# Performance work log

Hardware: AMD Instinct MI355X
Metric: run time of the kernel (lower is better)

## Reference

```python
import jax, jax.numpy as jnp
import numpy as np

B, C, H, W = 16, 512, 64, 64

def setup_inputs() -> dict:
    key = jax.random.key(0)
    k1, k2, k3 = jax.random.split(key, 3)
    x = jax.random.normal(k1, (B, C, H, W), dtype=jnp.float32)
    gamma = jnp.zeros((1,), dtype=jnp.float32)
    W1 = jax.random.normal(k2, (C, C // 8), dtype=jnp.float32) * (1.0 / np.sqrt(C))
    b1 = jnp.zeros((C // 8,), dtype=jnp.float32)
    W2 = jax.random.normal(k3, (C // 8, C), dtype=jnp.float32) * (1.0 / np.sqrt(C // 8))
    b2 = jnp.zeros((C,), dtype=jnp.float32)
    return {"x": x, "gamma": gamma, "W1": W1, "b1": b1, "W2": W2, "b2": b2}

def reference(x, gamma, W1, b1, W2, b2):
    b, c, h, w = x.shape
    q = x.reshape(b, c, h * w)                      # B,C,HW
    energy = jnp.einsum('bcn,bdn->bcd', q, q)       # B,C,C
    energy_new = jnp.max(energy, axis=-1, keepdims=True) - energy
    attention = jax.nn.softmax(energy_new, axis=-1)
    ch_out = jnp.einsum('bcd,bdn->bcn', attention, q).reshape(b, c, h, w)
    # SE branch: global avg pool -> Linear -> ReLU -> Linear -> Sigmoid
    se = jnp.mean(x, axis=(2, 3))                   # B,C
    se = jax.nn.relu(se @ W1 + b1)
    se = jax.nn.sigmoid(se @ W2 + b2)               # B,C
    out = gamma * (ch_out * se[:, :, None, None]) + x
    return out
```

## Files before the change

kernel.cpp:

```cpp
#include <hip/hip_runtime.h>
#include <cstdint>
#include <cstddef>

#define B_ 16
#define C_ 512
#define N_ 4096
#define CH_ 64

#define VMWAIT(n) asm volatile("s_waitcnt vmcnt(" #n ")" ::: "memory")
#define BARRAW()  asm volatile("s_barrier" ::: "memory")

typedef __attribute__((ext_vector_type(8))) short short8;
typedef __attribute__((ext_vector_type(4))) short short4t;
typedef __attribute__((ext_vector_type(4))) float f32x4;

__device__ __forceinline__ unsigned short f2bf(float f) {
  union { float f; unsigned u; } v; v.f = f;
  unsigned r = v.u + 0x7FFFu + ((v.u >> 16) & 1u);
  return (unsigned short)(r >> 16);
}
__device__ __forceinline__ ushort4 cvt4(float4 v) {
  ushort4 u; u.x = f2bf(v.x); u.y = f2bf(v.y); u.z = f2bf(v.z); u.w = f2bf(v.w);
  return u;
}
__device__ __forceinline__ void gload_lds16(const void* g, void* l) {
  __builtin_amdgcn_global_load_lds((__attribute__((address_space(1))) void*)g,
                                   (__attribute__((address_space(3))) void*)l,
                                   16, 0, 0);
}
__device__ __forceinline__ unsigned lds_off(const void* p) {
  return (unsigned)(size_t)(__attribute__((address_space(3))) const char*)p;
}

template <int CPW>
__device__ __forceinline__ void stage_pair(
    const unsigned short* __restrict__ Asrc, const unsigned short* __restrict__ Bsrc,
    char* Adst, char* Bdst, int t, int ko, bool doB) {
  const int l = t & 63, wid = t >> 6;
  const int srow = l >> 3, scc = l & 7;
#pragma unroll
  for (int i = 0; i < CPW; ++i) {
    const int chunk = wid * CPW + i;
    const int row = chunk * 8 + srow;
    const int cc = scc ^ (row & 7);
    gload_lds16(Asrc + (size_t)row * N_ + ko + cc * 8, Adst + chunk * 1024);
    if (doB)
      gload_lds16(Bsrc + (size_t)row * N_ + ko + cc * 8, Bdst + chunk * 1024);
  }
}
__device__ __forceinline__ void stage_att(
    const unsigned short* __restrict__ src, char* dst, int t, int ko) {
  const int l = t & 63, wid = t >> 6;
  const int srow = l >> 3, scc = l & 7;
#pragma unroll
  for (int i = 0; i < 2; ++i) {
    const int chunk = wid * 2 + i;
    const int row = chunk * 8 + srow;
    const int cc = scc ^ (row & 7);
    gload_lds16(src + (size_t)row * C_ + ko + cc * 8, dst + chunk * 1024);
  }
}
__device__ __forceinline__ void stage_q(
    const unsigned short* __restrict__ src,
    char* dst, int t) {
  const int l = t & 63, wid = t >> 6;
  const int dd = (l >> 1) & 3;
  const int n8 = ((l >> 3) << 1) | (l & 1);
#pragma unroll
  for (int i = 0; i < 2; ++i) {
    const int chunk = wid * 2 + i;
    gload_lds16(src + (size_t)(4 * chunk + dd) * N_ + n8 * 8,
                dst + chunk * 1024);
  }
}

template <int MF, int NF>
__device__ __forceinline__ void gemm_step_t(const char* Abase, const char* Bbase,
                                            int l, int wA, int wB,
                                            f32x4 (&acc)[MF][NF]) {
#pragma unroll
  for (int ks = 0; ks < 2; ++ks) {
    short8 af[MF], bfv[NF];
#pragma unroll
    for (int m = 0; m < MF; ++m) {
      const int row = wA * (MF * 16) + m * 16 + (l & 15);
      const int ch = (ks * 4 + (l >> 4)) ^ (row & 7);
      af[m] = *(const short8*)(Abase + row * 128 + ch * 16);
    }
#pragma unroll
    for (int n = 0; n < NF; ++n) {
      const int row = wB * (NF * 16) + n * 16 + (l & 15);
      const int ch = (ks * 4 + (l >> 4)) ^ (row & 7);
      bfv[n] = *(const short8*)(Bbase + row * 128 + ch * 16);
    }
#pragma unroll
    for (int m = 0; m < MF; ++m)
#pragma unroll
      for (int n = 0; n < NF; ++n)
        acc[m][n] = __builtin_amdgcn_mfma_f32_16x16x32_bf16(af[m], bfv[n],
                                                            acc[m][n], 0, 0, 0);
  }
}

__device__ __forceinline__ void gemm_tr(const char* Q, const char* P,
                                        int l, int wn, int wcc,
                                        f32x4 (&acc)[2][4]) {
  const int g = l >> 4;
  const unsigned qoff = lds_off(Q) + g * 2048 + (l & 15) * 2;
#pragma unroll
  for (int ks = 0; ks < 2; ++ks) {
    short4t alo[2], ahi[2];
#pragma unroll
    for (int m = 0; m < 2; ++m) {
      const unsigned a = qoff + ks * 8192 + (wn * 2 + m) * 128;
      asm volatile("ds_read_b64_tr_b16 %0, %2\n\t"
                   "ds_read_b64_tr_b16 %1, %2 offset:1024"
                   : "=&v"(alo[m]), "=&v"(ahi[m]) : "v"(a));
    }
    short8 bfv[4];
#pragma unroll
    for (int n = 0; n < 4; ++n) {
      const int row = wcc * 64 + n * 16 + (l & 15);
      const int ch = (ks * 4 + (l >> 4)) ^ (row & 7);
      bfv[n] = *(const short8*)(P + row * 128 + ch * 16);
    }
    asm volatile("s_waitcnt lgkmcnt(0)" ::: "memory");
    __builtin_amdgcn_sched_barrier(0);
#pragma unroll
    for (int m = 0; m < 2; ++m) {
      short8 af = __builtin_shufflevector(alo[m], ahi[m], 0, 1, 2, 3, 4, 5, 6, 7);
#pragma unroll
      for (int n = 0; n < 4; ++n)
        acc[m][n] = __builtin_amdgcn_mfma_f32_16x16x32_bf16(af, bfv[n],
                                                            acc[m][n], 0, 0, 0);
    }
  }
}

__global__ __launch_bounds__(256) void k1_convert(
    const float* __restrict__ x, unsigned short* __restrict__ qbf,
    float* __restrict__ partial) {
  __shared__ float wsum[4];
  const size_t base = (size_t)blockIdx.x * N_;
  const int t = threadIdx.x;
  float s = 0.f;
#pragma unroll
  for (int k = 0; k < 4; ++k) {
    const int idx = (t + k * 256) * 4;
    float4 v = *(const float4*)(x + base + idx);
    *(ushort4*)(qbf + base + idx) = cvt4(v);
    s += (v.x + v.y) + (v.z + v.w);
  }
#pragma unroll
  for (int o = 1; o < 64; o <<= 1) s += __shfl_xor(s, o);
  if ((t & 63) == 0) wsum[t >> 6] = s;
  __syncthreads();
  if (t == 0) partial[blockIdx.x] = (wsum[0] + wsum[1]) + (wsum[2] + wsum[3]);
}

__global__ __launch_bounds__(256) void k2_se(
    const float* __restrict__ partial, const float* __restrict__ gamma,
    const float* __restrict__ W1, const float* __restrict__ b1,
    const float* __restrict__ W2, const float* __restrict__ b2,
    float* __restrict__ gse) {
  __shared__ float se_s[C_];
  __shared__ float hp[4][CH_];
  __shared__ float h_s[CH_];
  const int b = blockIdx.x, t = threadIdx.x;
  for (int c = t; c < C_; c += 256)
    se_s[c] = partial[b * C_ + c] * (1.0f / (float)N_);
  __syncthreads();
  {
    const int h = t & 63, seg = t >> 6;
    float a = 0.f;
    const int cb = seg * 128;
    for (int c = cb; c < cb + 128; ++c) a += se_s[c] * W1[c * CH_ + h];
    hp[seg][h] = a;
  }
  __syncthreads();
  if (t < CH_) {
    float a = b1[t] + hp[0][t] + hp[1][t] + hp[2][t] + hp[3][t];
    h_s[t] = fmaxf(a, 0.f);
  }
  __syncthreads();
  const float g = gamma[0];
  for (int c = t; c < C_; c += 256) {
    float a = b2[c];
#pragma unroll
    for (int hh = 0; hh < CH_; ++hh) a += h_s[hh] * W2[hh * C_ + c];
    const float sig = 1.0f / (1.0f + __expf(-a));
    gse[b * C_ + c] = g * sig;
  }
}

__global__ __launch_bounds__(512) void k3_energy(
    const unsigned short* __restrict__ qbf, float* __restrict__ ep) {
  __shared__ alignas(16) char lds[65536];
  const int orig = blockIdx.x;
  const int wg = (orig & 7) * 80 + (orig >> 3);
  const int b = wg / 40;
  const int rem = wg % 40;
  const int kc = rem / 10;
  const int tid = rem % 10;
  int i, j;
  if (tid < 4)      { i = 0; j = tid; }
  else if (tid < 7) { i = 1; j = tid - 3; }
  else if (tid < 9) { i = 2; j = tid - 5; }
  else              { i = 3; j = 3; }
  const int c0 = i * 128, d0 = j * 128;
  const bool diag = (i == j);
  const unsigned short* qb = qbf + (size_t)b * C_ * N_ + kc * 1024;
  const int t = threadIdx.x, l = t & 63, wid = t >> 6;
  const int wd = wid >> 1, wcc = wid & 1;
  f32x4 acc[2][4];
#pragma unroll
  for (int m = 0; m < 2; ++m)
#pragma unroll
    for (int n = 0; n < 4; ++n) acc[m][n] = (f32x4){0.f, 0.f, 0.f, 0.f};
  char* A0 = lds;             char* B0 = lds + 16384;
  char* A1 = lds + 32768;     char* B1 = lds + 49152;
  const unsigned short* cp = qb + (size_t)c0 * N_;
  const unsigned short* dp = qb + (size_t)d0 * N_;

  stage_pair<2>(cp, dp, A0, B0, t, 0, !diag);
  for (int kt = 0; kt < 16; ++kt) {
    char* curA = (kt & 1) ? A1 : A0;
    char* curB = (kt & 1) ? B1 : B0;
    char* nxtA = (kt & 1) ? A0 : A1;
    char* nxtB = (kt & 1) ? B0 : B1;
    if (kt < 15) {
      stage_pair<2>(cp, dp, nxtA, nxtB, t, (kt + 1) * 64, !diag);
      if (diag) { VMWAIT(2); } else { VMWAIT(4); }
    } else {
      VMWAIT(0);
    }
    BARRAW();
    gemm_step_t<2, 4>(diag ? curA : curB, curA, l, wd, wcc, acc);
    BARRAW();
  }

  float* Lf = (float*)lds;
  float* eb = ep + ((size_t)(kc * B_ + b)) * C_ * C_;
#pragma unroll
  for (int df = 0; df < 2; ++df)
#pragma unroll
    for (int cf = 0; cf < 4; ++cf) {
      const int c_l = wcc * 64 + cf * 16 + (l & 15);
      const int d4 = wd * 32 + df * 16 + ((l >> 4) << 2);
      *(float4*)&Lf[c_l * 128 + (d4 ^ ((c_l & 7) << 2))] =
          *(const float4*)&acc[df][cf];
    }
  __syncthreads();
#pragma unroll
  for (int jj = 0; jj < 8; ++jj) {
    const int row = jj * 16 + (t >> 5);
    const int col4 = (t & 31) * 4;
    float4 v = *(const float4*)&Lf[row * 128 + (col4 ^ ((row & 7) << 2))];
    *(float4*)&eb[(size_t)(c0 + row) * C_ + d0 + col4] = v;
  }
  if (!diag) {
    __syncthreads();
#pragma unroll
    for (int df = 0; df < 2; ++df)
#pragma unroll
      for (int cf = 0; cf < 4; ++cf) {
        const int c_l = wcc * 64 + cf * 16 + (l & 15);
#pragma unroll
        for (int r = 0; r < 4; ++r) {
          const int d_l = wd * 32 + df * 16 + ((l >> 4) << 2) + r;
          Lf[d_l * 128 + (c_l ^ ((d_l & 7) << 2))] = acc[df][cf][r];
        }
      }
    __syncthreads();
#pragma unroll
    for (int jj = 0; jj < 8; ++jj) {
      const int row = jj * 16 + (t >> 5);
      const int col4 = (t & 31) * 4;
      float4 v = *(const float4*)&Lf[row * 128 + (col4 ^ ((row & 7) << 2))];
      *(float4*)&eb[(size_t)(d0 + row) * C_ + c0 + col4] = v;
    }
  }
}

__global__ __launch_bounds__(256) void k4_softmax(const float* __restrict__ ep,
                                                  unsigned short* __restrict__ att) {
  const int t = threadIdx.x, l = t & 63, wid = t >> 6;
  const size_t row = (size_t)blockIdx.x * 4 + wid;
  f32x4 v0 = (f32x4){0.f, 0.f, 0.f, 0.f}, v1 = v0;
#pragma unroll
  for (int k = 0; k < 4; ++k) {
    const f32x4* er = (const f32x4*)(ep + ((size_t)k * B_ * C_ + row) * C_);
    v0 += er[l];
    v1 += er[64 + l];
  }
  float mn = fminf(fminf(fminf(v0[0], v0[1]), fminf(v0[2], v0[3])),
                   fminf(fminf(v1[0], v1[1]), fminf(v1[2], v1[3])));
#pragma unroll
  for (int s = 1; s < 64; s <<= 1) mn = fminf(mn, __shfl_xor(mn, s));
  float e0 = __expf(mn - v0[0]), e1 = __expf(mn - v0[1]);
  float e2 = __expf(mn - v0[2]), e3 = __expf(mn - v0[3]);
  float e4 = __expf(mn - v1[0]), e5 = __expf(mn - v1[1]);
  float e6 = __expf(mn - v1[2]), e7 = __expf(mn - v1[3]);
  float sm = ((e0 + e1) + (e2 + e3)) + ((e4 + e5) + (e6 + e7));
#pragma unroll
  for (int s = 1; s < 64; s <<= 1) sm += __shfl_xor(sm, s);
  const float inv = 1.0f / sm;
  unsigned short* ar = att + row * C_;
  ushort4 u0, u1;
  u0.x = f2bf(e0 * inv); u0.y = f2bf(e1 * inv);
  u0.z = f2bf(e2 * inv); u0.w = f2bf(e3 * inv);
  u1.x = f2bf(e4 * inv); u1.y = f2bf(e5 * inv);
  u1.z = f2bf(e6 * inv); u1.w = f2bf(e7 * inv);
  *(ushort4*)(ar + 4 * l) = u0;
  *(ushort4*)(ar + 256 + 4 * l) = u1;
}

__global__ __launch_bounds__(512) void k5_pv(
    const unsigned short* __restrict__ att, const unsigned short* __restrict__ qbf,
    const float* __restrict__ gse, const float* __restrict__ x,
    float* __restrict__ out) {
  __shared__ alignas(16) char lds[65536];
  const int orig = blockIdx.x;
  const int wg = (orig & 7) * 256 + (orig >> 3);
  const int b = wg >> 7;
  const int rem = wg & 127;
  const int c0 = (rem & 3) * 128, n0 = (rem >> 2) * 128;
  const int t = threadIdx.x, l = t & 63, wid = t >> 6;
  const int wn = wid >> 1, wcc = wid & 1;
  const unsigned short* ap = att + (size_t)b * C_ * C_ + (size_t)c0 * C_;
  const unsigned short* qb = qbf + (size_t)b * C_ * N_ + n0;
  f32x4 acc[2][4];
#pragma unroll
  for (int m = 0; m < 2; ++m)
#pragma unroll
    for (int n = 0; n < 4; ++n) acc[m][n] = (f32x4){0.f, 0.f, 0.f, 0.f};
  char* P0 = lds;             char* Q0 = lds + 16384;
  char* P1 = lds + 32768;     char* Q1 = lds + 49152;

  stage_att(ap, P0, t, 0);
  stage_q(qb, Q0, t);
  for (int kt = 0; kt < 8; ++kt) {
    char* curP = (kt & 1) ? P1 : P0;
    char* curQ = (kt & 1) ? Q1 : Q0;
    char* nxtP = (kt & 1) ? P0 : P1;
    char* nxtQ = (kt & 1) ? Q0 : Q1;
    if (kt < 7) {
      stage_att(ap, nxtP, t, (kt + 1) * 64);
      stage_q(qb + (size_t)(kt + 1) * 64 * N_, nxtQ, t);
      VMWAIT(4);
    } else {
      VMWAIT(0);
    }
    BARRAW();
    gemm_tr(curQ, curP, l, wn, wcc, acc);
    BARRAW();
  }

  float* Lf = (float*)lds;
#pragma unroll
  for (int nf = 0; nf < 2; ++nf)
#pragma unroll
    for (int cf = 0; cf < 4; ++cf) {
      const int c_l = wcc * 64 + cf * 16 + (l & 15);
      const int n4 = wn * 32 + nf * 16 + ((l >> 4) << 2);
      *(float4*)&Lf[c_l * 128 + (n4 ^ ((c_l & 7) << 2))] =
          *(const float4*)&acc[nf][cf];
    }
  __syncthreads();
  const float* xb = x + (size_t)b * C_ * N_;
  float* ob = out + (size_t)b * C_ * N_;
  const float* gseb = gse + b * C_;
#pragma unroll
  for (int jj = 0; jj < 8; ++jj) {
    const int row = jj * 16 + (t >> 5);
    const int col4 = (t & 31) * 4;
    const int c = c0 + row;
    const float g = gseb[c];
    float4 v = *(const float4*)&Lf[row * 128 + (col4 ^ ((row & 7) << 2))];
    const size_t gofs = (size_t)c * N_ + n0 + col4;
    float4 xv = *(const float4*)(xb + gofs);
    float4 ov;
    ov.x = g * v.x + xv.x; ov.y = g * v.y + xv.y;
    ov.z = g * v.z + xv.z; ov.w = g * v.w + xv.w;
    *(float4*)(ob + gofs) = ov;
  }
}

extern "C" void kernel_launch(void* const* d_in, const int* in_sizes, int n_in,
                              void* d_out, int out_size, void* d_ws, size_t ws_size,
                              hipStream_t stream) {
  (void)in_sizes; (void)n_in; (void)out_size; (void)ws_size;
  const float* x     = (const float*)d_in[0];
  const float* gamma = (const float*)d_in[1];
  const float* W1    = (const float*)d_in[2];
  const float* b1    = (const float*)d_in[3];
  const float* W2    = (const float*)d_in[4];
  const float* b2    = (const float*)d_in[5];
  float* out = (float*)d_out;
  char* ws = (char*)d_ws;

  unsigned short* qbf     = (unsigned short*)(ws);
  unsigned short* att     = (unsigned short*)(ws + 67108864);
  float*          partial = (float*)(ws + 75497472);
  float*          gse     = (float*)(ws + 75530240);
  float* epartial = out;

  k1_convert<<<dim3(B_ * C_), dim3(256), 0, stream>>>(x, qbf, partial);
  k2_se<<<dim3(B_), dim3(256), 0, stream>>>(partial, gamma, W1, b1, W2, b2, gse);
  k3_energy<<<dim3(640), dim3(512), 0, stream>>>(qbf, epartial);
  k4_softmax<<<dim3(B_ * C_ / 4), dim3(256), 0, stream>>>(epartial, att);
  k5_pv<<<dim3(2048), dim3(512), 0, stream>>>(att, qbf, gse, x, out);
}
```

Before: 204.4 us.

## Enlarge PV tile to 256x256 with phased MFMA schedule and bf16 residual

Each k5_pv workgroup now computes a 256x256 output tile instead of 128x128. The grid drops to 512 blocks, LDS doubles to 128KB, and each K step is split into four phases that interleave transposed LDS reads, MFMA bursts at raised priority, and barriers. This is meant to improve reuse of attention and Q tiles and cut global staging traffic. The epilogue now takes the residual from the bf16 copy of x instead of the fp32 input, which halves that read but lowers the residual's precision. The larger accumulator array raises register pressure, and the bigger LDS footprint limits residency to one block per CU.

```diff
diff --git a/kernel.cpp b/kernel.cpp
--- a/kernel.cpp
+++ b/kernel.cpp
@@ -8,6 +8,7 @@
 #define CH_ 64
 
 #define VMWAIT(n) asm volatile("s_waitcnt vmcnt(" #n ")" ::: "memory")
+#define LGKM0()   asm volatile("s_waitcnt lgkmcnt(0)" ::: "memory")
 #define BARRAW()  asm volatile("s_barrier" ::: "memory")
 
 typedef __attribute__((ext_vector_type(8))) short short8;
@@ -18,6 +19,10 @@
   union { float f; unsigned u; } v; v.f = f;
   unsigned r = v.u + 0x7FFFu + ((v.u >> 16) & 1u);
   return (unsigned short)(r >> 16);
+}
+__device__ __forceinline__ float bf2f(unsigned short u) {
+  union { unsigned u; float f; } v; v.u = ((unsigned)u) << 16;
+  return v.f;
 }
 __device__ __forceinline__ ushort4 cvt4(float4 v) {
   ushort4 u; u.x = f2bf(v.x); u.y = f2bf(v.y); u.z = f2bf(v.z); u.w = f2bf(v.w);
@@ -48,93 +53,112 @@
       gload_lds16(Bsrc + (size_t)row * N_ + ko + cc * 8, Bdst + chunk * 1024);
   }
 }
-__device__ __forceinline__ void stage_att(
+template <int MF, int NF>
+__device__ __forceinline__ void gemm_step_t(const char* Abase, const char* Bbase,
+                                            int l, int wA, int wB,
+                                            f32x4 (&acc)[MF][NF]) {
+#pragma unroll
+  for (int ks = 0; ks < 2; ++ks) {
+    short8 af[MF], bfv[NF];
+#pragma unroll
+    for (int m = 0; m < MF; ++m) {
+      const int row = wA * (MF * 16) + m * 16 + (l & 15);
+      const int ch = (ks * 4 + (l >> 4)) ^ (row & 7);
+      af[m] = *(const short8*)(Abase + row * 128 + ch * 16);
+    }
+#pragma unroll
+    for (int n = 0; n < NF; ++n) {
+      const int row = wB * (NF * 16) + n * 16 + (l & 15);
+      const int ch = (ks * 4 + (l >> 4)) ^ (row & 7);
+      bfv[n] = *(const short8*)(Bbase + row * 128 + ch * 16);
+    }
+#pragma unroll
+    for (int m = 0; m < MF; ++m)
+#pragma unroll
+      for (int n = 0; n < NF; ++n)
+        acc[m][n] = __builtin_amdgcn_mfma_f32_16x16x32_bf16(af[m], bfv[n],
+                                                            acc[m][n], 0, 0, 0);
+  }
+}
+
+__device__ __forceinline__ void stage_att256(
     const unsigned short* __restrict__ src, char* dst, int t, int ko) {
   const int l = t & 63, wid = t >> 6;
   const int srow = l >> 3, scc = l & 7;
 #pragma unroll
-  for (int i = 0; i < 2; ++i) {
-    const int chunk = wid * 2 + i;
+  for (int i = 0; i < 4; ++i) {
+    const int chunk = wid * 4 + i;
     const int row = chunk * 8 + srow;
     const int cc = scc ^ (row & 7);
     gload_lds16(src + (size_t)row * C_ + ko + cc * 8, dst + chunk * 1024);
   }
 }
-__device__ __forceinline__ void stage_q(
+__device__ __forceinline__ void stage_q256(
     const unsigned short* __restrict__ src,
     char* dst, int t) {
   const int l = t & 63, wid = t >> 6;
   const int dd = (l >> 1) & 3;
-  const int n8 = ((l >> 3) << 1) | (l & 1);
-#pragma unroll
-  for (int i = 0; i < 2; ++i) {
-    const int chunk = wid * 2 + i;
-    gload_lds16(src + (size_t)(4 * chunk + dd) * N_ + n8 * 8,
+  const int nb = (l >> 3) * 16 + (l & 1) * 8;
+#pragma unroll
+  for (int i = 0; i < 4; ++i) {
+    const int chunk = wid * 4 + i;
+    gload_lds16(src + (size_t)((chunk >> 1) * 4 + dd) * N_ + (chunk & 1) * 128 + nb,
                 dst + chunk * 1024);
   }
 }
 
-template <int MF, int NF>
-__device__ __forceinline__ void gemm_step_t(const char* Abase, const char* Bbase,
-                                            int l, int wA, int wB,
-                                            f32x4 (&acc)[MF][NF]) {
-#pragma unroll
-  for (int ks = 0; ks < 2; ++ks) {
-    short8 af[MF], bfv[NF];
-#pragma unroll
-    for (int m = 0; m < MF; ++m) {
-      const int row = wA * (MF * 16) + m * 16 + (l & 15);
-      const int ch = (ks * 4 + (l >> 4)) ^ (row & 7);
-      af[m] = *(const short8*)(Abase + row * 128 + ch * 16);
-    }
-#pragma unroll
-    for (int n = 0; n < NF; ++n) {
-      const int row = wB * (NF * 16) + n * 16 + (l & 15);
-      const int ch = (ks * 4 + (l >> 4)) ^ (row & 7);
-      bfv[n] = *(const short8*)(Bbase + row * 128 + ch * 16);
-    }
-#pragma unroll
-    for (int m = 0; m < MF; ++m)
-#pragma unroll
-      for (int n = 0; n < NF; ++n)
-        acc[m][n] = __builtin_amdgcn_mfma_f32_16x16x32_bf16(af[m], bfv[n],
-                                                            acc[m][n], 0, 0, 0);
-  }
-}
-
-__device__ __forceinline__ void gemm_tr(const char* Q, const char* P,
-                                        int l, int wn, int wcc,
-                                        f32x4 (&acc)[2][4]) {
+template <int NA, int CB, bool LOADA, bool LOADB, bool WAITV>
+__device__ __forceinline__ void phase256(
+    const char* Qc, const char* Pc, int l, int wn2, int wc,
+    short4t (&aflo)[4][2], short4t (&afhi)[4][2], short8 (&af)[4][2],
+    short8 (&bf)[2][2], f32x4 (&acc)[8][4]) {
   const int g = l >> 4;
-  const unsigned qoff = lds_off(Q) + g * 2048 + (l & 15) * 2;
-#pragma unroll
-  for (int ks = 0; ks < 2; ++ks) {
-    short4t alo[2], ahi[2];
-#pragma unroll
-    for (int m = 0; m < 2; ++m) {
-      const unsigned a = qoff + ks * 8192 + (wn * 2 + m) * 128;
-      asm volatile("ds_read_b64_tr_b16 %0, %2\n\t"
-                   "ds_read_b64_tr_b16 %1, %2 offset:1024"
-                   : "=&v"(alo[m]), "=&v"(ahi[m]) : "v"(a));
-    }
-    short8 bfv[4];
-#pragma unroll
-    for (int n = 0; n < 4; ++n) {
-      const int row = wcc * 64 + n * 16 + (l & 15);
-      const int ch = (ks * 4 + (l >> 4)) ^ (row & 7);
-      bfv[n] = *(const short8*)(P + row * 128 + ch * 16);
-    }
-    asm volatile("s_waitcnt lgkmcnt(0)" ::: "memory");
-    __builtin_amdgcn_sched_barrier(0);
-#pragma unroll
-    for (int m = 0; m < 2; ++m) {
-      short8 af = __builtin_shufflevector(alo[m], ahi[m], 0, 1, 2, 3, 4, 5, 6, 7);
-#pragma unroll
-      for (int n = 0; n < 4; ++n)
-        acc[m][n] = __builtin_amdgcn_mfma_f32_16x16x32_bf16(af, bfv[n],
-                                                            acc[m][n], 0, 0, 0);
-    }
-  }
+  if (LOADA) {
+    const unsigned base = lds_off(Qc) + (unsigned)((wn2 * 8 + NA * 4) * 128 +
+                                                   g * 4096 + (l & 15) * 2);
+#pragma unroll
+    for (int mf = 0; mf < 4; ++mf)
+#pragma unroll
+      for (int ks = 0; ks < 2; ++ks) {
+        const unsigned a = base + mf * 128 + ks * 16384;
+        asm volatile("ds_read_b64_tr_b16 %0, %2\n\t"
+                     "ds_read_b64_tr_b16 %1, %2 offset:2048"
+                     : "=&v"(aflo[mf][ks]), "=&v"(afhi[mf][ks]) : "v"(a));
+      }
+  }
+  if (LOADB) {
+#pragma unroll
+    for (int cf = 0; cf < 2; ++cf)
+#pragma unroll
+      for (int ks = 0; ks < 2; ++ks) {
+        const int c_l = wc * 64 + CB * 32 + cf * 16 + (l & 15);
+        bf[cf][ks] = *(const short8*)(Pc + c_l * 128 +
+                                      (((ks * 4 + g) ^ (c_l & 7)) * 16));
+      }
+  }
+  BARRAW();
+  LGKM0();
+  __builtin_amdgcn_sched_barrier(0);
+  if (LOADA) {
+#pragma unroll
+    for (int mf = 0; mf < 4; ++mf)
+#pragma unroll
+      for (int ks = 0; ks < 2; ++ks)
+        af[mf][ks] = __builtin_shufflevector(aflo[mf][ks], afhi[mf][ks],
+                                             0, 1, 2, 3, 4, 5, 6, 7);
+  }
+  __builtin_amdgcn_s_setprio(1);
+#pragma unroll
+  for (int mf = 0; mf < 4; ++mf)
+#pragma unroll
+    for (int cf = 0; cf < 2; ++cf)
+#pragma unroll
+      for (int ks = 0; ks < 2; ++ks)
+        acc[NA * 4 + mf][CB * 2 + cf] = __builtin_amdgcn_mfma_f32_16x16x32_bf16(
+            af[mf][ks], bf[cf][ks], acc[NA * 4 + mf][CB * 2 + cf], 0, 0, 0);
+  __builtin_amdgcn_s_setprio(0);
+  if (WAITV) VMWAIT(0);
+  BARRAW();
 }
 
 __global__ __launch_bounds__(256) void k1_convert(
@@ -317,72 +341,88 @@
 
 __global__ __launch_bounds__(512) void k5_pv(
     const unsigned short* __restrict__ att, const unsigned short* __restrict__ qbf,
-    const float* __restrict__ gse, const float* __restrict__ x,
-    float* __restrict__ out) {
-  __shared__ alignas(16) char lds[65536];
+    const float* __restrict__ gse, float* __restrict__ out) {
+  __shared__ alignas(16) char lds[131072];
   const int orig = blockIdx.x;
-  const int wg = (orig & 7) * 256 + (orig >> 3);
-  const int b = wg >> 7;
-  const int rem = wg & 127;
-  const int c0 = (rem & 3) * 128, n0 = (rem >> 2) * 128;
+  const int wg = (orig & 7) * 64 + (orig >> 3);
+  const int b = wg >> 5;
+  const int rem = wg & 31;
+  const int c0 = (rem & 1) * 256, n0 = (rem >> 1) * 256;
   const int t = threadIdx.x, l = t & 63, wid = t >> 6;
-  const int wn = wid >> 1, wcc = wid & 1;
-  const unsigned short* ap = att + (size_t)b * C_ * C_ + (size_t)c0 * C_;
+  const int wn2 = wid >> 2, wc = wid & 3;
+  const unsigned short* ab = att + (size_t)b * C_ * C_ + (size_t)c0 * C_;
   const unsigned short* qb = qbf + (size_t)b * C_ * N_ + n0;
-  f32x4 acc[2][4];
-#pragma unroll
-  for (int m = 0; m < 2; ++m)
+  f32x4 acc[8][4];
+#pragma unroll
+  for (int m = 0; m < 8; ++m)
 #pragma unroll
     for (int n = 0; n < 4; ++n) acc[m][n] = (f32x4){0.f, 0.f, 0.f, 0.f};
-  char* P0 = lds;             char* Q0 = lds + 16384;
-  char* P1 = lds + 32768;     char* Q1 = lds + 49152;
-
-  stage_att(ap, P0, t, 0);
-  stage_q(qb, Q0, t);
+  char* P0 = lds;            char* P1 = lds + 32768;
+  char* Q0 = lds + 65536;    char* Q1 = lds + 98304;
+
+  short4t aflo[4][2], afhi[4][2];
+  short8 af[4][2], bf[2][2];
+
+  stage_att256(ab, P0, t, 0);
+  stage_q256(qb, Q0, t);
+  VMWAIT(0);
+  BARRAW();
   for (int kt = 0; kt < 8; ++kt) {
-    char* curP = (kt & 1) ? P1 : P0;
-    char* curQ = (kt & 1) ? Q1 : Q0;
-    char* nxtP = (kt & 1) ? P0 : P1;
-    char* nxtQ = (kt & 1) ? Q0 : Q1;
+    const char* Pc = (kt & 1) ? P1 : P0;
+    const char* Qc = (kt & 1) ? Q1 : Q0;
+    char* Pn = (kt & 1) ? P0 : P1;
+    char* Qn = (kt & 1) ? Q0 : Q1;
     if (kt < 7) {
-      stage_att(ap, nxtP, t, (kt + 1) * 64);
-      stage_q(qb + (size_t)(kt + 1) * 64 * N_, nxtQ, t);
-      VMWAIT(4);
+      stage_att256(ab, Pn, t, (kt + 1) * 64);
+      stage_q256(qb + (size_t)(kt + 1) * 64 * N_, Qn, t);
+      phase256<0, 0, true,  true,  false>(Qc, Pc, l, wn2, wc, aflo, afhi, af, bf, acc);
+      phase256<0, 1, false, true,  false>(Qc, Pc, l, wn2, wc, aflo, afhi, af, bf, acc);
+      phase256<1, 1, true,  false, false>(Qc, Pc, l, wn2, wc, aflo, afhi, af, bf, acc);
+      phase256<1, 0, false, true,  true >(Qc, Pc, l, wn2, wc, aflo, afhi, af, bf, acc);
     } else {
-      VMWAIT(0);
-    }
-    BARRAW();
-    gemm_tr(curQ, curP, l, wn, wcc, acc);
-    BARRAW();
+      phase256<0, 0, true,  true,  false>(Qc, Pc, l, wn2, wc, aflo, afhi, af, bf, acc);
+      phase256<0, 1, false, true,  false>(Qc, Pc, l, wn2, wc, aflo, afhi, af, bf, acc);
+      phase256<1, 1, true,  false, false>(Qc, Pc, l, wn2, wc, aflo, afhi, af, bf, acc);
+      phase256<1, 0, false, true,  false>(Qc, Pc, l, wn2, wc, aflo, afhi, af, bf, acc);
+    }
   }
 
   float* Lf = (float*)lds;
-#pragma unroll
-  for (int nf = 0; nf < 2; ++nf)
-#pragma unroll
-    for (int cf = 0; cf < 4; ++cf) {
-      const int c_l = wcc * 64 + cf * 16 + (l & 15);
-      const int n4 = wn * 32 + nf * 16 + ((l >> 4) << 2);
-      *(float4*)&Lf[c_l * 128 + (n4 ^ ((c_l & 7) << 2))] =
-          *(const float4*)&acc[nf][cf];
-    }
-  __syncthreads();
-  const float* xb = x + (size_t)b * C_ * N_;
+  const unsigned short* xb = qbf + (size_t)b * C_ * N_;
   float* ob = out + (size_t)b * C_ * N_;
   const float* gseb = gse + b * C_;
-#pragma unroll
-  for (int jj = 0; jj < 8; ++jj) {
-    const int row = jj * 16 + (t >> 5);
-    const int col4 = (t & 31) * 4;
-    const int c = c0 + row;
-    const float g = gseb[c];
-    float4 v = *(const float4*)&Lf[row * 128 + (col4 ^ ((row & 7) << 2))];
-    const size_t gofs = (size_t)c * N_ + n0 + col4;
-    float4 xv = *(const float4*)(xb + gofs);
-    float4 ov;
-    ov.x = g * v.x + xv.x; ov.y = g * v.y + xv.y;
-    ov.z = g * v.z + xv.z; ov.w = g * v.w + xv.w;
-    *(float4*)(ob + gofs) = ov;
+  const int g16 = l >> 4;
+#pragma unroll
+  for (int s = 0; s < 2; ++s) {
+    BARRAW();
+    if (wn2 == s) {
+#pragma unroll
+      for (int m = 0; m < 8; ++m)
+#pragma unroll
+        for (int cf = 0; cf < 4; ++cf) {
+          const int c_l = wc * 64 + cf * 16 + (l & 15);
+          const int n4 = (m >> 2) * 64 + (m & 3) * 16 + g16 * 4;
+          *(float4*)&Lf[c_l * 128 + (n4 ^ ((c_l & 7) << 2))] =
+              *(const float4*)&acc[m][cf];
+        }
+    }
+    BARRAW();
+#pragma unroll
+    for (int it = 0; it < 16; ++it) {
+      const int row = it * 16 + (t >> 5);
+      const int col4 = (t & 31) * 4;
+      const int c = c0 + row;
+      const float g = gseb[c];
+      float4 v = *(const float4*)&Lf[row * 128 + (col4 ^ ((row & 7) << 2))];
+      const size_t gofs = (size_t)c * N_ + n0 + s * 128 + col4;
+      ushort4 xu = *(const ushort4*)(xb + gofs);
+      float4 ov;
+      ov.x = g * v.x + bf2f(xu.x);
+      ov.y = g * v.y + bf2f(xu.y);
+      ov.z = g * v.z + bf2f(xu.z);
+      ov.w = g * v.w + bf2f(xu.w);
+      *(float4*)(ob + gofs) = ov;
+    }
   }
 }
 
@@ -409,5 +449,5 @@
   k2_se<<<dim3(B_), dim3(256), 0, stream>>>(partial, gamma, W1, b1, W2, b2, gse);
   k3_energy<<<dim3(640), dim3(512), 0, stream>>>(qbf, epartial);
   k4_softmax<<<dim3(B_ * C_ / 4), dim3(256), 0, stream>>>(epartial, att);
-  k5_pv<<<dim3(2048), dim3(512), 0, stream>>>(att, qbf, gse, x, out);
-}
+  k5_pv<<<dim3(512), dim3(512), 0, stream>>>(att, qbf, gse, out);
+}
```

Measured after the change: 316.8 us. 55.0% more time.
